# Kernel tuning notes

Measured on AMD Instinct MI355X. Metric: run time of the kernel, lower is better.

Reference implementation:

```python
import jax, jax.numpy as jnp
import numpy as np

B, T, D, H = 4, 2048, 1024, 16
HD = D // H  # 64


def setup_inputs() -> dict:
    key = jax.random.key(0)
    ks = jax.random.split(key, 6)
    s = 0.02
    return {
        "embed": jax.random.normal(ks[0], (B, T, D), dtype=jnp.float32),
        "mask": jnp.ones((1, 1, 1, T), dtype=jnp.int32),
        "Wq": jax.random.normal(ks[1], (D, D), dtype=jnp.float32) * s,
        "bq": jnp.zeros((D,), dtype=jnp.float32),
        "Wk": jax.random.normal(ks[2], (D, D), dtype=jnp.float32) * s,
        "bk": jnp.zeros((D,), dtype=jnp.float32),
        "Wv": jax.random.normal(ks[3], (D, D), dtype=jnp.float32) * s,
        "bv": jnp.zeros((D,), dtype=jnp.float32),
        "Wo": jax.random.normal(ks[4], (D, D), dtype=jnp.float32) * s,
        "bo": jnp.zeros((D,), dtype=jnp.float32),
    }


def _attn(embed, Wq, bq, Wk, bk, Wv, bv, Wo, bo, mask):
    b, t, _ = embed.shape
    q = (embed @ Wq + bq).reshape(b, t, H, HD).transpose(0, 2, 1, 3)  # [B,H,T,hd]
    k = (embed @ Wk + bk).reshape(b, t, H, HD).transpose(0, 2, 1, 3)
    v = (embed @ Wv + bv).reshape(b, t, H, HD).transpose(0, 2, 1, 3)
    scores = jnp.einsum("bhqd,bhkd->bhqk", q, k) * (1.0 / np.sqrt(HD))
    scores = jnp.where(mask == 0, jnp.float32(-jnp.inf), scores)
    weights = jax.nn.softmax(scores, axis=-1)  # dropout p=0 in eval
    ctx = jnp.einsum("bhqk,bhkd->bhqd", weights, v)
    merged = ctx.transpose(0, 2, 1, 3).reshape(b, t, D)
    return merged @ Wo + bo


def reference(embed, mask, Wq, bq, Wk, bk, Wv, bv, Wo, bo):
    return _attn(embed, Wq, bq, Wk, bk, Wv, bv, Wo, bo, mask)
```

## Files before the change

kernel.cpp:

```cpp
#include <hip/hip_runtime.h>


typedef __bf16 bf16_t;
typedef bf16_t bf16x8 __attribute__((ext_vector_type(8)));
typedef float  f32x4  __attribute__((ext_vector_type(4)));
typedef unsigned u32x4 __attribute__((ext_vector_type(4)));
typedef unsigned short u16x8 __attribute__((ext_vector_type(8)));
typedef unsigned short u16x4 __attribute__((ext_vector_type(4)));

#define DEV static __device__ __forceinline__

constexpr int Bc = 4, Tc = 2048, Dc = 1024, Hc = 16, HDc = 64;
constexpr int Mc = Bc * Tc;
constexpr int NQKV = 3 * Dc;

DEV unsigned short f2bf(float f) {
  union { float f; unsigned u; } v; v.f = f;
  return (unsigned short)((v.u + 0x7fffu + ((v.u >> 16) & 1u)) >> 16);
}

DEV void gload_lds16(const void* g, const void* ldsbase) {
  unsigned m0v = __builtin_amdgcn_readfirstlane((unsigned)(unsigned long long)ldsbase);
  asm volatile("s_mov_b32 m0, %0\n\t"
               "global_load_lds_dwordx4 %1, off"
               :: "s"(m0v), "v"(g) : "memory");
}

DEV f32x4 mfma16(bf16x8 a, bf16x8 b, f32x4 c) {
  return __builtin_amdgcn_mfma_f32_16x16x32_bf16(a, b, c, 0, 0, 0);
}

DEV void pl32swap(unsigned& a, unsigned& b) {
  asm("v_permlane32_swap_b32 %0, %1" : "+v"(a), "+v"(b));
}
DEV void pl16swap(unsigned& a, unsigned& b) {
  asm("v_permlane16_swap_b32 %0, %1" : "+v"(a), "+v"(b));
}

DEV int fragaddr(int row, int col) {
  return (row >> 4) * 1024 + ((col >> 5) << 9) + (((col >> 3) & 3) << 7)
       + ((row & 15) << 3) + (col & 7);
}

__global__ __launch_bounds__(256) void prep(const float* __restrict__ embed,
                                            const float* __restrict__ Wq,
                                            const float* __restrict__ Wk,
                                            const float* __restrict__ Wv,
                                            const float* __restrict__ Wo,
                                            const float* __restrict__ bq,
                                            const float* __restrict__ bk,
                                            const float* __restrict__ bv,
                                            unsigned short* __restrict__ embed_bf,
                                            unsigned short* __restrict__ WtAll,
                                            float* __restrict__ ball) {
  __shared__ unsigned short tile[64 * 80];
  const int bb = blockIdx.x;
  const int tid = threadIdx.x;

  if (bb < 8192) {
    int i = bb * 256 + tid;
    float4 v = ((const float4*)embed)[i];
    u16x4 o = { f2bf(v.x), f2bf(v.y), f2bf(v.z), f2bf(v.w) };
    *(u16x4*)(embed_bf + (size_t)i * 4) = o;
    return;
  }
  if (bb < 8192 + 1024) {
    int wb = bb - 8192;
    int bx = wb & 15, by = (wb >> 4) & 15, bz = wb >> 8;
    const float* W = bz == 0 ? Wq : bz == 1 ? Wk : bz == 2 ? Wv : Wo;
    unsigned short* dst = WtAll + (size_t)bz * 1024 * 1024;
    const int kb = by * 64, nb = bx * 64;
#pragma unroll
    for (int i = 0; i < 4; i++) {
      int ci = i * 256 + tid;
      int r = ci >> 4, c4 = ci & 15;
      float4 v = *(const float4*)(W + (size_t)(kb + r) * 1024 + nb + c4 * 4);
      u16x4 o = { f2bf(v.x), f2bf(v.y), f2bf(v.z), f2bf(v.w) };
      *(u16x4*)(tile + r * 80 + c4 * 4) = o;
    }
    __syncthreads();
#pragma unroll
    for (int i = 0; i < 2; i++) {
      int ci = i * 256 + tid;
      int n = ci >> 3, c8 = ci & 7;
      u16x8 o;
#pragma unroll
      for (int j = 0; j < 8; j++) o[j] = tile[(c8 * 8 + j) * 80 + n];
      *(u16x8*)(dst + (size_t)(nb + n) * 1024 + kb + c8 * 8) = o;
    }
    return;
  }
#pragma unroll
  for (int it = 0; it < 12; it++) {
    int i = it * 256 + tid;
    ball[i] = (i < 1024) ? bq[i] : (i < 2048) ? bk[i - 1024] : bv[i - 2048];
  }
}

__global__ __launch_bounds__(512, 2) void gemm_qkv11(
    const unsigned short* __restrict__ Wt,
    const unsigned short* __restrict__ Eb,
    const float* __restrict__ bias,
    unsigned short* __restrict__ Qf,
    unsigned short* __restrict__ Kf,
    unsigned short* __restrict__ Vf) {
  __shared__ unsigned short As_[4 * 8192];
  __shared__ unsigned short Bs_[4 * 8192];

  const int tid = threadIdx.x;
  const int lane = tid & 63, wid = tid >> 6;
  const int lr = lane & 15, lg = lane >> 4;
  const int wr = wid >> 2, wc = wid & 3;

  const int lin = blockIdx.y * 12 + blockIdx.x;
  const int swz = (lin & 7) * 48 + (lin >> 3);
  const int m0 = (swz % 12) * 256, n0 = (swz / 12) * 256;

  size_t gA[2], gB[2];
  int ldsoff[2];
#pragma unroll
  for (int i = 0; i < 2; i++) {
    int ci = i * 512 + tid;
    int row = ci >> 2;
    int cl = (ci & 3) ^ ((row ^ (row >> 2)) & 3);
    gA[i] = (size_t)(m0 + row) * 1024 + cl * 8;
    gB[i] = (size_t)(n0 + row) * 1024 + cl * 8;
    ldsoff[i] = ci * 8;
  }

  int offA[2][4], offB[4];
#pragma unroll
  for (int mq = 0; mq < 2; mq++)
#pragma unroll
    for (int m = 0; m < 4; m++) {
      int row = wr * 128 + mq * 64 + m * 16 + lr;
      offA[mq][m] = row * 32 + ((lg ^ ((row ^ (row >> 2)) & 3)) << 3);
    }
#pragma unroll
  for (int n = 0; n < 4; n++) {
    int row = wc * 64 + n * 16 + lr;
    offB[n] = row * 32 + ((lg ^ ((row ^ (row >> 2)) & 3)) << 3);
  }

  f32x4 acc[8][4] = {};

#define QSTAGE(kt) {                                                         \
    const int sbi_ = (kt) & 3;                                               \
    _Pragma("unroll")                                                        \
    for (int i_ = 0; i_ < 2; i_++) {                                         \
      gload_lds16(Wt + gA[i_] + (size_t)(kt) * 32,                           \
                  As_ + sbi_ * 8192 + ldsoff[i_]);                           \
      gload_lds16(Eb + gB[i_] + (size_t)(kt) * 32,                           \
                  Bs_ + sbi_ * 8192 + ldsoff[i_]);                           \
    } }

#define QKTILE(kt, VM, DOST) {                                               \
    const int bi_ = (kt) & 3;                                                \
    const unsigned short* Ab = As_ + bi_ * 8192;                             \
    const unsigned short* Bb = Bs_ + bi_ * 8192;                             \
    asm volatile("s_waitcnt vmcnt(" VM ")" ::: "memory");                    \
    asm volatile("s_barrier" ::: "memory");                                  \
    bf16x8 a0 = *(const bf16x8*)(Ab + offA[0][0]);                           \
    bf16x8 a1 = *(const bf16x8*)(Ab + offA[0][1]);                           \
    bf16x8 a2 = *(const bf16x8*)(Ab + offA[0][2]);                           \
    bf16x8 a3 = *(const bf16x8*)(Ab + offA[0][3]);                           \
    bf16x8 b0 = *(const bf16x8*)(Bb + offB[0]);                              \
    bf16x8 b1 = *(const bf16x8*)(Bb + offB[1]);                              \
    bf16x8 b2 = *(const bf16x8*)(Bb + offB[2]);                              \
    bf16x8 b3 = *(const bf16x8*)(Bb + offB[3]);                              \
    if (DOST) QSTAGE((kt) + 3);                                              \
    __builtin_amdgcn_s_setprio(1);                                           \
    acc[0][0]=mfma16(a0,b0,acc[0][0]); acc[0][1]=mfma16(a0,b1,acc[0][1]);    \
    acc[0][2]=mfma16(a0,b2,acc[0][2]); acc[0][3]=mfma16(a0,b3,acc[0][3]);    \
    acc[1][0]=mfma16(a1,b0,acc[1][0]); acc[1][1]=mfma16(a1,b1,acc[1][1]);    \
    acc[1][2]=mfma16(a1,b2,acc[1][2]); acc[1][3]=mfma16(a1,b3,acc[1][3]);    \
    acc[2][0]=mfma16(a2,b0,acc[2][0]); acc[2][1]=mfma16(a2,b1,acc[2][1]);    \
    acc[2][2]=mfma16(a2,b2,acc[2][2]); acc[2][3]=mfma16(a2,b3,acc[2][3]);    \
    acc[3][0]=mfma16(a3,b0,acc[3][0]); acc[3][1]=mfma16(a3,b1,acc[3][1]);    \
    acc[3][2]=mfma16(a3,b2,acc[3][2]); acc[3][3]=mfma16(a3,b3,acc[3][3]);    \
    __builtin_amdgcn_s_setprio(0);                                           \
    a0 = *(const bf16x8*)(Ab + offA[1][0]);                                  \
    a1 = *(const bf16x8*)(Ab + offA[1][1]);                                  \
    a2 = *(const bf16x8*)(Ab + offA[1][2]);                                  \
    a3 = *(const bf16x8*)(Ab + offA[1][3]);                                  \
    __builtin_amdgcn_s_setprio(1);                                           \
    acc[4][0]=mfma16(a0,b0,acc[4][0]); acc[4][1]=mfma16(a0,b1,acc[4][1]);    \
    acc[4][2]=mfma16(a0,b2,acc[4][2]); acc[4][3]=mfma16(a0,b3,acc[4][3]);    \
    acc[5][0]=mfma16(a1,b0,acc[5][0]); acc[5][1]=mfma16(a1,b1,acc[5][1]);    \
    acc[5][2]=mfma16(a1,b2,acc[5][2]); acc[5][3]=mfma16(a1,b3,acc[5][3]);    \
    acc[6][0]=mfma16(a2,b0,acc[6][0]); acc[6][1]=mfma16(a2,b1,acc[6][1]);    \
    acc[6][2]=mfma16(a2,b2,acc[6][2]); acc[6][3]=mfma16(a2,b3,acc[6][3]);    \
    acc[7][0]=mfma16(a3,b0,acc[7][0]); acc[7][1]=mfma16(a3,b1,acc[7][1]);    \
    acc[7][2]=mfma16(a3,b2,acc[7][2]); acc[7][3]=mfma16(a3,b3,acc[7][3]);    \
    __builtin_amdgcn_s_setprio(0); }

  QSTAGE(0); QSTAGE(1); QSTAGE(2);

#pragma unroll 1
  for (int kt = 0; kt < 29; ++kt) {
    QKTILE(kt, "8", 1);
  }
  QKTILE(29, "8", 0);
  QKTILE(30, "4", 0);
  QKTILE(31, "0", 0);
#undef QSTAGE
#undef QKTILE

  const int ft = m0 >> 8;
  if (ft < 8) {
#pragma unroll
    for (int g = 0; g < 2; g++) {
      const int fb = m0 + wr * 128 + g * 64;
      const bool isQ = (fb < Dc);
      unsigned short* const dstm = isQ ? Qf : Kf;
      const int head = (isQ ? fb : fb - Dc) >> 6;
      float4 b4[4];
#pragma unroll
      for (int mq = 0; mq < 4; mq++)
        b4[mq] = *(const float4*)(bias + fb + mq * 16 + lg * 4);
#pragma unroll
      for (int n = 0; n < 4; n++) {
        unsigned w8[4][2];
#pragma unroll
        for (int mq = 0; mq < 4; mq++) {
          float e0 = acc[g * 4 + mq][n][0] + b4[mq].x;
          float e1 = acc[g * 4 + mq][n][1] + b4[mq].y;
          float e2 = acc[g * 4 + mq][n][2] + b4[mq].z;
          float e3 = acc[g * 4 + mq][n][3] + b4[mq].w;
          if (isQ) {
            e0 *= 0.18033688f; e1 *= 0.18033688f;
            e2 *= 0.18033688f; e3 *= 0.18033688f;
          }
          asm("v_cvt_pk_bf16_f32 %0, %1, %2" : "=v"(w8[mq][0]) : "v"(e0), "v"(e1));
          asm("v_cvt_pk_bf16_f32 %0, %1, %2" : "=v"(w8[mq][1]) : "v"(e2), "v"(e3));
        }
        const int t = n0 + wc * 64 + n * 16;
        const int bb = t >> 11, tl = t & 2047;
        unsigned short* dst = dstm + (size_t)(bb * 16 + head) * 131072
                            + (tl >> 4) * 1024;
#pragma unroll
        for (int half = 0; half < 2; half++) {
          unsigned a0 = w8[2 * half][0], c0 = w8[2 * half + 1][0];
          unsigned a1 = w8[2 * half][1], c1 = w8[2 * half + 1][1];
          pl32swap(a0, c0);
          pl32swap(a1, c1);
          pl16swap(a0, c0);
          pl16swap(a1, c1);
          u32x4 w = { a0, a1, c0, c1 };
          *(u32x4*)(dst + half * 512 + lane * 8) = w;
        }
      }
    }
  } else {
#pragma unroll
    for (int m = 0; m < 8; m++)
#pragma unroll
      for (int n = 0; n < 4; n++)
#pragma unroll
        for (int r = 0; r < 4; r++) {
          int f = m0 + wr * 128 + m * 16 + lg * 4 + r;
          int t = n0 + wc * 64 + n * 16 + lr;
          float v = acc[m][n][r] + bias[f];
          int c = f - 2 * Dc, head = c >> 6, d = c & 63;
          int bb = t >> 11, tl = t & 2047;
          Vf[(size_t)(bb * 16 + head) * 131072 + (tl >> 6) * 4096
             + fragaddr(d, tl & 63)] = f2bf(v);
        }
  }
}

__global__ __launch_bounds__(256) void gemm_bt(const unsigned short* __restrict__ A,
                                               const unsigned short* __restrict__ Bt,
                                               const float* __restrict__ bias,
                                               float* __restrict__ Cout,
                                               int N, int K) {
  __shared__ unsigned short As[128 * 64];
  __shared__ unsigned short Bs[128 * 64];
  const int tid = threadIdx.x;
  const int lane = tid & 63, wid = tid >> 6;
  const int lr = lane & 15, lg = lane >> 4;
  const int wrow = wid >> 1, wcol = wid & 1;
  const int m0 = blockIdx.y * 128, n0 = blockIdx.x * 128;

  f32x4 acc[4][4] = {};

  for (int k0 = 0; k0 < K; k0 += 64) {
#pragma unroll
    for (int i = 0; i < 4; i++) {
      int ci = i * 256 + tid;
      int row = ci >> 3, ph = ci & 7;
      int cl = ph ^ (row & 7);
      gload_lds16(A + (size_t)(m0 + row) * K + k0 + cl * 8, As + (size_t)(i * 256 + wid * 64) * 8);
      gload_lds16(Bt + (size_t)(n0 + row) * K + k0 + cl * 8, Bs + (size_t)(i * 256 + wid * 64) * 8);
    }
    asm volatile("s_waitcnt vmcnt(0)" ::: "memory");
    __syncthreads();
#pragma unroll
    for (int kk = 0; kk < 2; kk++) {
      bf16x8 av[4], bv[4];
#pragma unroll
      for (int m = 0; m < 4; m++) {
        int row = wrow * 64 + m * 16 + lr;
        int ph = (kk * 4 + lg) ^ (row & 7);
        av[m] = *(const bf16x8*)(As + row * 64 + ph * 8);
      }
#pragma unroll
      for (int n = 0; n < 4; n++) {
        int row = wcol * 64 + n * 16 + lr;
        int ph = (kk * 4 + lg) ^ (row & 7);
        bv[n] = *(const bf16x8*)(Bs + row * 64 + ph * 8);
      }
#pragma unroll
      for (int m = 0; m < 4; m++)
#pragma unroll
        for (int n = 0; n < 4; n++)
          acc[m][n] = mfma16(av[m], bv[n], acc[m][n]);
    }
    __syncthreads();
  }

#pragma unroll
  for (int m = 0; m < 4; m++)
#pragma unroll
    for (int n = 0; n < 4; n++)
#pragma unroll
      for (int r = 0; r < 4; r++) {
        int row = m0 + wrow * 64 + m * 16 + lg * 4 + r;
        int col = n0 + wcol * 64 + n * 16 + lr;
        Cout[(size_t)row * N + col] = acc[m][n][r] + bias[col];
      }
}

__global__ __launch_bounds__(256, 2) void flash7(const unsigned short* __restrict__ Qf,
                                                 const unsigned short* __restrict__ Kf,
                                                 const unsigned short* __restrict__ Vf,
                                                 const int* __restrict__ mask,
                                                 unsigned short* __restrict__ merged) {
  const int tid = threadIdx.x;
  const int lane = tid & 63, wid = tid >> 6;
  const int lr = lane & 15, lg = lane >> 4;

  const int lin = blockIdx.y * 8 + blockIdx.x;
  const int swz = (lin & 7) * 64 + (lin >> 3);
  const int qb = swz & 7, bh = swz >> 3;
  const int b = bh >> 4, h = bh & 15;
  const int wq = qb * 256 + wid * 64;

  const unsigned short* Qb = Qf + (size_t)bh * 131072;
  const unsigned short* Kb = Kf + (size_t)bh * 131072;
  const unsigned short* Vb = Vf + (size_t)bh * 131072;

  bf16x8 qf[4][2];
#pragma unroll
  for (int qn = 0; qn < 4; qn++)
#pragma unroll
    for (int kk = 0; kk < 2; kk++)
      qf[qn][kk] = *(const bf16x8*)(Qb + ((wq >> 4) + qn) * 1024 + kk * 512 + lane * 8);

  f32x4 o[4][4] = {};
  f32x4 lacc[4] = {};

  bf16x8 ones;
#pragma unroll
  for (int j = 0; j < 8; j++) ones[j] = (bf16_t)1.0f;

  bool allone = true;
#pragma unroll
  for (int j = 0; j < 8; j++) {
    int4 mv = ((const int4*)mask)[j * 64 + lane];
    allone = allone && (mv.x != 0) && (mv.y != 0) && (mv.z != 0) && (mv.w != 0);
  }
  const bool nomask = (__ballot(allone) == ~0ull);

#pragma unroll 2
  for (int tile = 0; tile < 32; tile++) {
    bf16x8 kf[4][2];
#pragma unroll
    for (int n = 0; n < 4; n++)
#pragma unroll
      for (int kk = 0; kk < 2; kk++)
        kf[n][kk] = *(const bf16x8*)(Kb + (tile * 4 + n) * 1024 + kk * 512 + lane * 8);
    bf16x8 vf[4][2];
#pragma unroll
    for (int dn = 0; dn < 4; dn++)
#pragma unroll
      for (int kk = 0; kk < 2; kk++)
        vf[dn][kk] = *(const bf16x8*)(Vb + tile * 4096 + dn * 1024 + kk * 512 + lane * 8);

    unsigned long long mb = ~0ull;
    if (!nomask) mb = __ballot(mask[tile * 64 + lane] != 0);

    unsigned pk[4][4][2];
#pragma unroll
    for (int kvn = 0; kvn < 4; kvn++) {
      f32x4 st[4] = {};
#pragma unroll
      for (int qn = 0; qn < 4; qn++) {
        st[qn] = mfma16(kf[kvn][0], qf[qn][0], st[qn]);
        st[qn] = mfma16(kf[kvn][1], qf[qn][1], st[qn]);
      }
      if (mb != ~0ull) {
#pragma unroll
        for (int r = 0; r < 4; r++)
          if (!((mb >> (kvn * 16 + lg * 4 + r)) & 1ull)) {
#pragma unroll
            for (int qn = 0; qn < 4; qn++) st[qn][r] = -1e30f;
          }
      }
#pragma unroll
      for (int qn = 0; qn < 4; qn++) {
        float e[4];
#pragma unroll
        for (int r = 0; r < 4; r++)
          asm("v_exp_f32 %0, %1" : "=v"(e[r]) : "v"(st[qn][r]));
        asm("v_cvt_pk_bf16_f32 %0, %1, %2" : "=v"(pk[qn][kvn][0]) : "v"(e[0]), "v"(e[1]));
        asm("v_cvt_pk_bf16_f32 %0, %1, %2" : "=v"(pk[qn][kvn][1]) : "v"(e[2]), "v"(e[3]));
      }
    }

    bf16x8 pa[4][2];
#pragma unroll
    for (int qn = 0; qn < 4; qn++)
#pragma unroll
      for (int m = 0; m < 2; m++) {
        unsigned a0 = pk[qn][2 * m][0], b0 = pk[qn][2 * m + 1][0];
        unsigned a1 = pk[qn][2 * m][1], b1 = pk[qn][2 * m + 1][1];
        pl32swap(a0, b0);
        pl32swap(a1, b1);
        pl16swap(a0, b0);
        pl16swap(a1, b1);
        u32x4 w = { a0, a1, b0, b1 };
        pa[qn][m] = __builtin_bit_cast(bf16x8, w);
      }

    __builtin_amdgcn_s_setprio(1);
#pragma unroll
    for (int qn = 0; qn < 4; qn++) {
#pragma unroll
      for (int dn = 0; dn < 4; dn++) {
        o[qn][dn] = mfma16(pa[qn][0], vf[dn][0], o[qn][dn]);
        o[qn][dn] = mfma16(pa[qn][1], vf[dn][1], o[qn][dn]);
      }
      lacc[qn] = mfma16(pa[qn][0], ones, lacc[qn]);
      lacc[qn] = mfma16(pa[qn][1], ones, lacc[qn]);
    }
    __builtin_amdgcn_s_setprio(0);
  }

#pragma unroll
  for (int qn = 0; qn < 4; qn++)
#pragma unroll
    for (int r = 0; r < 4; r++) {
      float inv = 1.0f / lacc[qn][r];
      int grow = b * Tc + wq + qn * 16 + lg * 4 + r;
#pragma unroll
      for (int dn = 0; dn < 4; dn++) {
        int gcol = h * HDc + dn * 16 + lr;
        merged[(size_t)grow * Dc + gcol] = f2bf(o[qn][dn][r] * inv);
      }
    }
}

extern "C" void kernel_launch(void* const* d_in, const int* in_sizes, int n_in,
                              void* d_out, int out_size, void* d_ws, size_t ws_size,
                              hipStream_t stream) {
  const float* embed = (const float*)d_in[0];
  const int*   mask  = (const int*)d_in[1];
  const float* Wq = (const float*)d_in[2];
  const float* bq = (const float*)d_in[3];
  const float* Wk = (const float*)d_in[4];
  const float* bk = (const float*)d_in[5];
  const float* Wv = (const float*)d_in[6];
  const float* bv = (const float*)d_in[7];
  const float* Wo = (const float*)d_in[8];
  const float* bo = (const float*)d_in[9];
  float* out = (float*)d_out;

  char* ws = (char*)d_ws;
  unsigned short* embed_bf = (unsigned short*)ws; ws += (size_t)Mc * Dc * 2;
  unsigned short* WtAll    = (unsigned short*)ws; ws += (size_t)4 * Dc * Dc * 2;
  float*          ball     = (float*)ws;          ws += 16384;
  unsigned short* Qf       = (unsigned short*)ws; ws += (size_t)Mc * Dc * 2;
  unsigned short* Kf       = (unsigned short*)ws; ws += (size_t)Mc * Dc * 2;
  unsigned short* Vf       = (unsigned short*)ws; ws += (size_t)Mc * Dc * 2;
  unsigned short* merged   = (unsigned short*)ws; ws += (size_t)Mc * Dc * 2;

  prep<<<8192 + 1024 + 1, 256, 0, stream>>>(embed, Wq, Wk, Wv, Wo, bq, bk, bv,
                                            embed_bf, WtAll, ball);
  gemm_qkv11<<<dim3(12, 32), 512, 0, stream>>>(WtAll, embed_bf, ball, Qf, Kf, Vf);
  flash7<<<dim3(8, 64), 256, 0, stream>>>(Qf, Kf, Vf, mask, merged);
  gemm_bt<<<dim3(8, 64), 256, 0, stream>>>(merged, WtAll + (size_t)3 * Dc * Dc, bo, out, Dc, Dc);
}
```

Measured before the change: 177.6 us.

## Split attention KV range across two halves with fp16 partials and reduce kernel

The flash kernel now splits the key/value sequence into two halves per query block, using 512-thread blocks with 512 queries each. Each half writes unnormalized fp16 partial outputs and row sums to workspace. A new reduce kernel adds the two halves, normalizes, and writes the bf16 merged tensor. This raises parallelism and shortens each block's serial KV loop, at the cost of extra global traffic, an extra launch, and fp16 partials that skip a max-subtraction step (the code has no running max, so it relies on bounded scores).

After: 628.6 us. 3.54x slower.

```diff
diff --git a/kernel.cpp b/kernel.cpp
--- a/kernel.cpp
+++ b/kernel.cpp
@@ -17,6 +17,15 @@
 DEV unsigned short f2bf(float f) {
   union { float f; unsigned u; } v; v.f = f;
   return (unsigned short)((v.u + 0x7fffu + ((v.u >> 16) & 1u)) >> 16);
+}
+
+DEV unsigned short f2h(float f) {
+  _Float16 h = (_Float16)f;
+  return __builtin_bit_cast(unsigned short, h);
+}
+DEV float h2f(unsigned short u) {
+  _Float16 h = __builtin_bit_cast(_Float16, u);
+  return (float)h;
 }
 
 DEV void gload_lds16(const void* g, const void* ldsbase) {
@@ -331,20 +340,21 @@
       }
 }
 
-__global__ __launch_bounds__(256, 2) void flash7(const unsigned short* __restrict__ Qf,
+__global__ __launch_bounds__(512, 4) void flash9(const unsigned short* __restrict__ Qf,
                                                  const unsigned short* __restrict__ Kf,
                                                  const unsigned short* __restrict__ Vf,
                                                  const int* __restrict__ mask,
-                                                 unsigned short* __restrict__ merged) {
+                                                 unsigned short* __restrict__ Opart,
+                                                 unsigned short* __restrict__ Lpart) {
   const int tid = threadIdx.x;
   const int lane = tid & 63, wid = tid >> 6;
   const int lr = lane & 15, lg = lane >> 4;
 
   const int lin = blockIdx.y * 8 + blockIdx.x;
   const int swz = (lin & 7) * 64 + (lin >> 3);
-  const int qb = swz & 7, bh = swz >> 3;
+  const int kvh = swz & 1, qb = (swz >> 1) & 3, bh = swz >> 3;
   const int b = bh >> 4, h = bh & 15;
-  const int wq = qb * 256 + wid * 64;
+  const int wq = qb * 512 + wid * 64;
 
   const unsigned short* Qb = Qf + (size_t)bh * 131072;
   const unsigned short* Kb = Kf + (size_t)bh * 131072;
@@ -372,8 +382,9 @@
   }
   const bool nomask = (__ballot(allone) == ~0ull);
 
+  const int t0 = kvh * 16, t1 = t0 + 16;
 #pragma unroll 2
-  for (int tile = 0; tile < 32; tile++) {
+  for (int tile = t0; tile < t1; tile++) {
     bf16x8 kf[4][2];
 #pragma unroll
     for (int n = 0; n < 4; n++)
@@ -447,18 +458,74 @@
     __builtin_amdgcn_s_setprio(0);
   }
 
+  const int c = (bh * 4 + qb) * 8 + wid;
+  unsigned short* ob = Opart + (size_t)c * 8192 + kvh * 4096 + lane * 64;
+#pragma unroll
+  for (int qn = 0; qn < 4; qn++) {
+    unsigned p[8];
+#pragma unroll
+    for (int dn = 0; dn < 4; dn++) {
+      asm("v_cvt_pkrtz_f16_f32 %0, %1, %2" : "=v"(p[dn * 2]) : "v"(o[qn][dn][0]), "v"(o[qn][dn][1]));
+      asm("v_cvt_pkrtz_f16_f32 %0, %1, %2" : "=v"(p[dn * 2 + 1]) : "v"(o[qn][dn][2]), "v"(o[qn][dn][3]));
+    }
+    u32x4 wlo = { p[0], p[1], p[2], p[3] };
+    u32x4 whi = { p[4], p[5], p[6], p[7] };
+    *(u32x4*)(ob + qn * 16) = wlo;
+    *(u32x4*)(ob + qn * 16 + 8) = whi;
+  }
+  if (lr == 0) {
+#pragma unroll
+    for (int qn = 0; qn < 4; qn++)
+#pragma unroll
+      for (int r = 0; r < 4; r++) {
+        int row = qn * 16 + lg * 4 + r;
+        Lpart[(size_t)c * 128 + kvh * 64 + row] = f2h(lacc[qn][r]);
+      }
+  }
+}
+
+__global__ __launch_bounds__(256) void reduce_o(const unsigned short* __restrict__ Opart,
+                                                const unsigned short* __restrict__ Lpart,
+                                                unsigned short* __restrict__ merged) {
+  const int t = blockIdx.x * 256 + threadIdx.x;
+  const int c = t >> 6, lane = t & 63;
+  const int bh = c >> 5, qb = (c >> 3) & 3, wid = c & 7;
+  const int b = bh >> 4, h = bh & 15;
+  const int lg = lane >> 4, lr = lane & 15;
+
+  const unsigned short* o0 = Opart + (size_t)c * 8192 + lane * 64;
+  const unsigned short* o1 = o0 + 4096;
+
+  float linv[16];
 #pragma unroll
   for (int qn = 0; qn < 4; qn++)
 #pragma unroll
     for (int r = 0; r < 4; r++) {
-      float inv = 1.0f / lacc[qn][r];
-      int grow = b * Tc + wq + qn * 16 + lg * 4 + r;
-#pragma unroll
-      for (int dn = 0; dn < 4; dn++) {
-        int gcol = h * HDc + dn * 16 + lr;
-        merged[(size_t)grow * Dc + gcol] = f2bf(o[qn][dn][r] * inv);
-      }
-    }
+      int row = qn * 16 + lg * 4 + r;
+      float l0 = h2f(Lpart[(size_t)c * 128 + row]);
+      float l1 = h2f(Lpart[(size_t)c * 128 + 64 + row]);
+      linv[qn * 4 + r] = 1.0f / (l0 + l1);
+    }
+
+#pragma unroll
+  for (int qn = 0; qn < 4; qn++) {
+    u16x8 a0 = *(const u16x8*)(o0 + qn * 16);
+    u16x8 a1 = *(const u16x8*)(o0 + qn * 16 + 8);
+    u16x8 c0 = *(const u16x8*)(o1 + qn * 16);
+    u16x8 c1 = *(const u16x8*)(o1 + qn * 16 + 8);
+#pragma unroll
+    for (int dn = 0; dn < 4; dn++)
+#pragma unroll
+      for (int r = 0; r < 4; r++) {
+        int j = dn * 4 + r;
+        unsigned short h0 = (j < 8) ? a0[j] : a1[j - 8];
+        unsigned short h1 = (j < 8) ? c0[j] : c1[j - 8];
+        float s = h2f(h0) + h2f(h1);
+        int q = qb * 512 + wid * 64 + qn * 16 + lg * 4 + r;
+        int d = dn * 16 + lr;
+        merged[((size_t)(b * 2048 + q)) * 1024 + h * 64 + d] = f2bf(s * linv[qn * 4 + r]);
+      }
+  }
 }
 
 extern "C" void kernel_launch(void* const* d_in, const int* in_sizes, int n_in,
@@ -477,17 +544,21 @@
   float* out = (float*)d_out;
 
   char* ws = (char*)d_ws;
-  unsigned short* embed_bf = (unsigned short*)ws; ws += (size_t)Mc * Dc * 2;
-  unsigned short* WtAll    = (unsigned short*)ws; ws += (size_t)4 * Dc * Dc * 2;
-  float*          ball     = (float*)ws;          ws += 16384;
-  unsigned short* Qf       = (unsigned short*)ws; ws += (size_t)Mc * Dc * 2;
-  unsigned short* Kf       = (unsigned short*)ws; ws += (size_t)Mc * Dc * 2;
-  unsigned short* Vf       = (unsigned short*)ws; ws += (size_t)Mc * Dc * 2;
-  unsigned short* merged   = (unsigned short*)ws; ws += (size_t)Mc * Dc * 2;
+  unsigned short* WtAll  = (unsigned short*)ws; ws += (size_t)4 * Dc * Dc * 2;
+  unsigned short* Qf     = (unsigned short*)ws; ws += (size_t)Mc * Dc * 2;
+  unsigned short* Kf     = (unsigned short*)ws; ws += (size_t)Mc * Dc * 2;
+  unsigned short* Vf     = (unsigned short*)ws; ws += (size_t)Mc * Dc * 2;
+  unsigned short* merged = (unsigned short*)ws; ws += (size_t)Mc * Dc * 2;
+  unsigned short* embed_bf = (unsigned short*)ws;
+  unsigned short* Opart    = embed_bf;          ws += (size_t)Mc * Dc * 2;
+  float*          ball     = (float*)ws;        ws += 16384;
+  ws += (size_t)2048 * 8192 * 2 - ((size_t)Mc * Dc * 2 + 16384);
+  unsigned short* Lpart  = (unsigned short*)ws; ws += (size_t)2048 * 128 * 2;
 
   prep<<<8192 + 1024 + 1, 256, 0, stream>>>(embed, Wq, Wk, Wv, Wo, bq, bk, bv,
                                             embed_bf, WtAll, ball);
   gemm_qkv11<<<dim3(12, 32), 512, 0, stream>>>(WtAll, embed_bf, ball, Qf, Kf, Vf);
-  flash7<<<dim3(8, 64), 256, 0, stream>>>(Qf, Kf, Vf, mask, merged);
+  flash9<<<dim3(8, 64), 512, 0, stream>>>(Qf, Kf, Vf, mask, Opart, Lpart);
+  reduce_o<<<512, 256, 0, stream>>>(Opart, Lpart, merged);
   gemm_bt<<<dim3(8, 64), 256, 0, stream>>>(merged, WtAll + (size_t)3 * Dc * Dc, bo, out, Dc, Dc);
 }
```
